# Kernel tuning notes

Measured on AMD Instinct MI355X. Metric: run time of the kernel, lower is better.

## Reference

```python
import jax, jax.numpy as jnp
import numpy as np

D_MODEL = 512
DQ = D_MODEL // 4  # 128
TIME_SHIFT_START = 256
VELOCITY_START = 768
NOTE_OFF_START = 128


def conv1d(x, w, b, stride, pad):
    # x: [B, Cin, L], w: [Cout, Cin, K]
    y = jax.lax.conv_general_dilated(x, w, (stride,), [(pad, pad)],
                                     dimension_numbers=('NCH', 'OIH', 'NCH'))
    return y + b[None, :, None]


def adaptive_avg_pool1d(x, out_size):
    # faithful to torch AdaptiveAvgPool1d bin boundaries
    L = x.shape[-1]
    starts = (np.arange(out_size) * L) // out_size
    ends = np.ceil((np.arange(out_size) + 1) * L / out_size).astype(np.int64)
    cs = jnp.concatenate([jnp.zeros(x.shape[:-1] + (1,), x.dtype),
                          jnp.cumsum(x, axis=-1)], axis=-1)
    return (cs[..., ends] - cs[..., starts]) / jnp.asarray(ends - starts, x.dtype)


def setup_inputs() -> dict:
    key = jax.random.key(0)
    ks = jax.random.split(key, 20)

    def w(k, shape):
        fan_in = int(np.prod(shape[1:]))
        return jax.random.normal(k, shape, jnp.float32) / np.sqrt(fan_in)

    def b(k, n):
        return jax.random.normal(k, (n,), jnp.float32) * 0.01

    return {
        'tokens': jax.random.randint(ks[0], (32, 4096), 0, 774),
        'r1_w': w(ks[1], (32, 1, 8)),    'r1_b': b(ks[2], 32),
        'r2_w': w(ks[3], (64, 32, 4)),   'r2_b': b(ks[4], 64),
        'h1_w': w(ks[5], (64, 128, 12)), 'h1_b': b(ks[6], 64),
        'h2_w': w(ks[7], (32, 64, 8)),   'h2_b': b(ks[8], 32),
        'm1_w': w(ks[9], (64, 128, 5)),  'm1_b': b(ks[10], 64),
        'm2_w': w(ks[11], (32, 64, 3)),  'm2_b': b(ks[12], 32),
        'd1_w': w(ks[13], (16, 6, 4)),   'd1_b': b(ks[14], 16),
        'd2_w': w(ks[15], (16, 16, 3)),  'd2_b': b(ks[16], 16),
        'fc_w': w(ks[17], (D_MODEL, D_MODEL)), 'fc_b': b(ks[18], D_MODEL),
    }


def reference(tokens, r1_w, r1_b, r2_w, r2_b, h1_w, h1_b, h2_w, h2_b,
              m1_w, m1_b, m2_w, m2_b, d1_w, d1_b, d2_w, d2_b, fc_w, fc_b):
    B, S = tokens.shape
    relu = jax.nn.relu

    # rhythm: binary time-shift indicator [B,1,S]
    ts = ((tokens >= TIME_SHIFT_START) & (tokens < VELOCITY_START)).astype(jnp.float32)[:, None, :]
    r = relu(conv1d(ts, r1_w, r1_b, 2, 3))
    r = relu(conv1d(r, r2_w, r2_b, 2, 1))
    r = adaptive_avg_pool1d(r, DQ).reshape(B, -1)  # [B, 64*DQ]

    # vectorized one-hot pitch scatter (replaces the python double loop): [B,128,S]
    nm = tokens < NOTE_OFF_START
    pitch = jnp.transpose(
        jax.nn.one_hot(jnp.where(nm, tokens, 0) % 128, 128, dtype=jnp.float32)
        * nm[..., None].astype(jnp.float32), (0, 2, 1))

    h = relu(conv1d(pitch, h1_w, h1_b, 1, 6))
    h = relu(conv1d(h, h2_w, h2_b, 2, 3))
    h = adaptive_avg_pool1d(h, DQ).reshape(B, -1)  # [B, 32*DQ]

    m = relu(conv1d(pitch, m1_w, m1_b, 1, 2))
    m = relu(conv1d(m, m2_w, m2_b, 1, 1))
    m = adaptive_avg_pool1d(m, DQ).reshape(B, -1)  # [B, 32*DQ]

    # velocity one-hot scatter: [B,6,S]
    vm = tokens >= VELOCITY_START
    vel = jnp.clip(jnp.where(vm, tokens - VELOCITY_START, 0), 0, 5)
    vpat = jnp.transpose(
        jax.nn.one_hot(vel, 6, dtype=jnp.float32) * vm[..., None].astype(jnp.float32),
        (0, 2, 1))
    d = relu(conv1d(vpat, d1_w, d1_b, 1, 2))
    d = relu(conv1d(d, d2_w, d2_b, 1, 1))
    d = adaptive_avg_pool1d(d, DQ).reshape(B, -1)  # [B, 16*DQ]

    # total flattened size is 36*d_model != d_model, so torch branch always pools
    r, h, m, d = [adaptive_avg_pool1d(f[:, None, :], DQ)[:, 0] for f in (r, h, m, d)]

    combined = jnp.concatenate([r, h, m, d], axis=1)       # [B, d_model]
    feats = combined @ fc_w.T + fc_b                        # Linear
    return jnp.broadcast_to(feats[:, None, :], (B, S, D_MODEL))
```

## Files before the change

### kernel.cpp

```cpp
#include <hip/hip_runtime.h>

typedef unsigned short u16;
typedef unsigned int u32;
typedef float vf4 __attribute__((ext_vector_type(4)));
typedef unsigned int vu4 __attribute__((ext_vector_type(4)));
typedef short sh8 __attribute__((ext_vector_type(8)));
typedef float f32x4 __attribute__((ext_vector_type(4)));

__device__ __forceinline__ float bf2f(u16 u) {
  return __uint_as_float(((u32)u) << 16);
}
__device__ __forceinline__ u16 f2bf(float f) {
  u32 x = __float_as_uint(f);
  return (u16)((x + 0x7fffu + ((x >> 16) & 1u)) >> 16);
}
__device__ __forceinline__ float ldin(const void* p, int idx, int isf) {
  return isf ? ((const float*)p)[idx] : bf2f(((const u16*)p)[idx]);
}

#define OFF_FLAG  ((size_t)0)
#define OFF_WB    ((size_t)16)
#define OFF_WTH1  ((size_t)1180432)
#define OFF_WTM1  ((size_t)1573648)
#define OFF_COMB  ((size_t)1737488)
#define OFF_FEATF ((size_t)1803024)
#define OFF_FEATB ((size_t)1868560)
#define OFF_DP    ((size_t)18686736)
#define OFF_WH2B  ((size_t)52536080)
#define OFF_WH2L  ((size_t)52568848)
#define OFF_WM2B  ((size_t)52601616)
#define OFF_WM2L  ((size_t)52613904)
#define WS_NEEDED ((size_t)52626192)

#define WB_R1W 0
#define WB_R1B 256
#define WB_R2W 288
#define WB_R2B 8480
#define WB_H1B 8544
#define WB_H2W 8608
#define WB_H2B 24992
#define WB_M1B 25024
#define WB_M2W 25088
#define WB_M2B 31232
#define WB_D1W 31264
#define WB_D1B 31648
#define WB_D2W 31664
#define WB_D2B 32432
#define WB_FCW 32448
#define WB_FCB 294592
#define WB_TOTAL 295104

__global__ __launch_bounds__(256) void k_convert(
    const void* r1_w, const void* r1_b, const void* r2_w, const void* r2_b,
    const void* h1_w, const void* h1_b, const void* h2_w, const void* h2_b,
    const void* m1_w, const void* m1_b, const void* m2_w, const void* m2_b,
    const void* d1_w, const void* d1_b, const void* d2_w, const void* d2_b,
    const void* fc_w, const void* fc_b,
    int* __restrict__ flagp, float* __restrict__ wb,
    float* __restrict__ wTh1, float* __restrict__ wTm1,
    float* __restrict__ combined,
    u16* __restrict__ wh2b, u16* __restrict__ wh2l,
    u16* __restrict__ wm2b, u16* __restrict__ wm2l) {
  __shared__ int cnt[4];
  int tid = threadIdx.x;
  {
    u16 v = ((const u16*)fc_w)[2 * tid];
    int e = (v >> 7) & 0xFF;
    int outside = (e < 100 || e > 140) ? 1 : 0;
    unsigned long long m = __ballot(outside);
    if ((tid & 63) == 0) cnt[tid >> 6] = __popcll(m);
  }
  __syncthreads();
  int isf = (cnt[0] + cnt[1] + cnt[2] + cnt[3] >= 64) ? 1 : 0;
  if (blockIdx.x == 0 && tid == 0) flagp[0] = isf;

  int j = blockIdx.x * 256 + tid;
  if (j >= 473280) return;
  if (j < WB_TOTAL) {
    const void* src; int si;
    if      (j < WB_R1B) { src = r1_w; si = j; }
    else if (j < WB_R2W) { src = r1_b; si = j - WB_R1B; }
    else if (j < WB_R2B) { src = r2_w; si = j - WB_R2W; }
    else if (j < WB_H1B) { src = r2_b; si = j - WB_R2B; }
    else if (j < WB_H2W) { src = h1_b; si = j - WB_H1B; }
    else if (j < WB_H2B) { src = h2_w; si = j - WB_H2W; }
    else if (j < WB_M1B) { src = h2_b; si = j - WB_H2B; }
    else if (j < WB_M2W) { src = m1_b; si = j - WB_M1B; }
    else if (j < WB_M2B) { src = m2_w; si = j - WB_M2W; }
    else if (j < WB_D1W) { src = m2_b; si = j - WB_M2B; }
    else if (j < WB_D1B) { src = d1_w; si = j - WB_D1W; }
    else if (j < WB_D2W) { src = d1_b; si = j - WB_D1B; }
    else if (j < WB_D2B) { src = d2_w; si = j - WB_D2W; }
    else if (j < WB_FCW) { src = d2_b; si = j - WB_D2B; }
    else if (j < WB_FCB) { src = fc_w; si = j - WB_FCW; }
    else                 { src = fc_b; si = j - WB_FCB; }
    wb[j] = ldin(src, si, isf);
  } else if (j < 393408) {
    int j2 = j - WB_TOTAL;
    int o = j2 & 63, r = j2 >> 6, k = r % 12, p = r / 12;
    wTh1[j2] = ldin(h1_w, (o * 128 + p) * 12 + k, isf);
  } else if (j < 434368) {
    int j3 = j - 393408;
    int o = j3 & 63, r = j3 >> 6, k = r % 5, p = r / 5;
    wTm1[j3] = ldin(m1_w, (o * 128 + p) * 5 + k, isf);
  } else if (j < 450752) {
    combined[j - 434368] = 0.f;
  } else if (j < 467136) {
    int jj = j - 450752;
    int o = jj >> 9, rem = jj & 511, c = rem >> 3, kk = rem & 7;
    float w = ldin(h2_w, (o * 64 + c) * 8 + kk, isf);
    u16 hi = f2bf(w);
    wh2b[jj] = hi;
    wh2l[jj] = f2bf(w - bf2f(hi));
  } else {
    int jj = j - 467136;
    int o = jj / 192, rem = jj % 192, c = rem / 3, kk = rem % 3;
    float w = ldin(m2_w, (o * 64 + c) * 3 + kk, isf);
    u16 hi = f2bf(w);
    wm2b[jj] = hi;
    wm2l[jj] = f2bf(w - bf2f(hi));
  }
}


#define HT_STRIDE 142
#define MT_STRIDE 265

__device__ __forceinline__ void dev_hf(float* smem, const int* tok,
                                       const float* wTh1, const float* h1bf,
                                       const u16* wh2b, const u16* wh2l,
                                       const float* h2bf,
                                       float* combined, int chunk, int q, int b) {
  u16* htile = (u16*)smem;
  int* tks = (int*)(smem + 4544);
  const int tid = threadIdx.x;
  const int tb = q * 512 + chunk * 64;
  const int sg0 = 2 * tb;
  const int* tokb = tok + b * 4096;
  if (tid < 146) {
    int x = sg0 - 9 + tid;
    tks[tid] = ((unsigned)x < 4096u) ? tokb[x] : 999;
  }
  __syncthreads();
  {
    const int og = tid & 15, slot = tid >> 4;
    const float4 bias = *(const float4*)(h1bf + og * 4);
    for (int pos = slot; pos < 134; pos += 16) {
      int t = sg0 - 3 + pos;
      u16 o0 = 0, o1 = 0, o2 = 0, o3 = 0;
      if ((unsigned)t <= 4096u) {
        float4 acc = bias;
#pragma unroll
        for (int k = 0; k < 12; ++k) {
          int p = tks[pos + k];
          if (p < 128) {
            float4 wv = *(const float4*)(wTh1 + (p * 12 + k) * 64 + og * 4);
            acc.x += wv.x; acc.y += wv.y; acc.z += wv.z; acc.w += wv.w;
          }
        }
        o0 = f2bf(fmaxf(acc.x, 0.f)); o1 = f2bf(fmaxf(acc.y, 0.f));
        o2 = f2bf(fmaxf(acc.z, 0.f)); o3 = f2bf(fmaxf(acc.w, 0.f));
      }
      int rb = og * 4 * HT_STRIDE + pos;
      htile[rb] = o0;
      htile[rb + HT_STRIDE] = o1;
      htile[rb + 2 * HT_STRIDE] = o2;
      htile[rb + 3 * HT_STRIDE] = o3;
    }
  }
  __syncthreads();
  const int w = tid >> 6, l = tid & 63;
  const int quad = l >> 4, n = l & 15;
  const int ot = w & 1, tp = w >> 1;
  f32x4 acc2[2];
  acc2[0] = (f32x4){0.f, 0.f, 0.f, 0.f};
  acc2[1] = (f32x4){0.f, 0.f, 0.f, 0.f};
  const u16* wph = wh2b + (size_t)(16 * ot + n) * 512 + quad * 8;
  const u16* wpl = wh2l + (size_t)(16 * ot + n) * 512 + quad * 8;
  const u32* hp = (const u32*)htile;
  for (int kc = 0; kc < 2; ++kc) {
    sh8 ah[8], al[8];
#pragma unroll
    for (int s = 0; s < 8; ++s) {
      ah[s] = *(const sh8*)(wph + kc * 256 + 32 * s);
      al[s] = *(const sh8*)(wpl + kc * 256 + 32 * s);
    }
#pragma unroll
    for (int it = 0; it < 2; ++it) {
      int fb = 16 * (2 * it + tp) + n;
#pragma unroll
      for (int s = 0; s < 8; ++s) {
        int c = kc * 32 + 4 * s + quad;
        const u32* p = hp + c * 71 + fb;
        u32 bw[4] = {p[0], p[1], p[2], p[3]};
        sh8 bb;
        __builtin_memcpy(&bb, bw, 16);
        acc2[it] = __builtin_amdgcn_mfma_f32_16x16x32_bf16(ah[s], bb, acc2[it], 0, 0, 0);
        acc2[it] = __builtin_amdgcn_mfma_f32_16x16x32_bf16(al[s], bb, acc2[it], 0, 0, 0);
      }
    }
  }
#pragma unroll
  for (int r = 0; r < 4; ++r) {
    float bsv = h2bf[16 * ot + quad * 4 + r];
    float s = fmaxf(acc2[0][r] + bsv, 0.f) + fmaxf(acc2[1][r] + bsv, 0.f);
    s += __shfl_xor(s, 1, 64);
    s += __shfl_xor(s, 2, 64);
    s += __shfl_xor(s, 4, 64);
    s += __shfl_xor(s, 8, 64);
    if (n == 0) {
      int o = 16 * ot + quad * 4 + r;
      atomicAdd(&combined[b * 512 + 128 + 4 * o + q], s * (1.f / 512.f));
    }
  }
}

__device__ __forceinline__ void dev_mf(float* smem, const int* tok,
                                       const float* wTm1, const float* m1bf,
                                       const u16* wm2b, const u16* wm2l,
                                       const float* m2bf,
                                       float* combined, int sub, int q, int b) {
  u16* mtile = (u16*)smem;
  int* tks = (int*)(smem + 8480);
  const int tid = threadIdx.x;
  const int tb = q * 1024 + sub * 256;
  const int* tokb = tok + b * 4096;
  for (int i = tid; i < 266; i += 256) {
    int x = tb - 4 + i;
    tks[i] = ((unsigned)x < 4096u) ? tokb[x] : 999;
  }
  __syncthreads();
  {
    const int og = tid & 15, slot = tid >> 4;
    const float4 bias = *(const float4*)(m1bf + og * 4);
    for (int u = slot; u < 262; u += 16) {
      int t = tb - 2 + u;
      u16 o0 = 0, o1 = 0, o2 = 0, o3 = 0;
      if ((unsigned)t < 4096u) {
        float4 acc = bias;
#pragma unroll
        for (int k = 0; k < 5; ++k) {
          int p = tks[u + k];
          if (p < 128) {
            float4 wv = *(const float4*)(wTm1 + (p * 5 + k) * 64 + og * 4);
            acc.x += wv.x; acc.y += wv.y; acc.z += wv.z; acc.w += wv.w;
          }
        }
        o0 = f2bf(fmaxf(acc.x, 0.f)); o1 = f2bf(fmaxf(acc.y, 0.f));
        o2 = f2bf(fmaxf(acc.z, 0.f)); o3 = f2bf(fmaxf(acc.w, 0.f));
      }
      int rb = og * 4 * MT_STRIDE + u;
      mtile[rb] = o0;
      mtile[rb + MT_STRIDE] = o1;
      mtile[rb + 2 * MT_STRIDE] = o2;
      mtile[rb + 3 * MT_STRIDE] = o3;
    }
  }
  __syncthreads();
  const int w = tid >> 6, l = tid & 63;
  const int quad = l >> 4, n = l & 15;
  const int ot = w & 1, tp = w >> 1;
  sh8 ah[6], al[6];
  {
    const u16* wph = wm2b + (size_t)(16 * ot + n) * 192 + quad * 8;
    const u16* wpl = wm2l + (size_t)(16 * ot + n) * 192 + quad * 8;
#pragma unroll
    for (int s = 0; s < 6; ++s) {
      ah[s] = *(const sh8*)(wph + 32 * s);
      al[s] = *(const sh8*)(wpl + 32 * s);
    }
  }
  float bsv[4];
#pragma unroll
  for (int r = 0; r < 4; ++r) bsv[r] = m2bf[16 * ot + quad * 4 + r];
  float sm[4] = {0.f, 0.f, 0.f, 0.f};
  const int gkb = quad * 8;
  for (int it = 0; it < 8; ++it) {
    int ub = 16 * (2 * it + tp) + n + 1;
    f32x4 acc = {0.f, 0.f, 0.f, 0.f};
#pragma unroll
    for (int s = 0; s < 6; ++s) {
      sh8 bb;
#pragma unroll
      for (int j = 0; j < 8; ++j) {
        int gk = 32 * s + gkb + j;
        int c = (gk * 21846) >> 16;
        int kk = gk - 3 * c;
        bb[j] = (short)mtile[c * MT_STRIDE + ub + kk];
      }
      acc = __builtin_amdgcn_mfma_f32_16x16x32_bf16(ah[s], bb, acc, 0, 0, 0);
      acc = __builtin_amdgcn_mfma_f32_16x16x32_bf16(al[s], bb, acc, 0, 0, 0);
    }
#pragma unroll
    for (int r = 0; r < 4; ++r) sm[r] += fmaxf(acc[r] + bsv[r], 0.f);
  }
#pragma unroll
  for (int r = 0; r < 4; ++r) {
    float s = sm[r];
    s += __shfl_xor(s, 1, 64);
    s += __shfl_xor(s, 2, 64);
    s += __shfl_xor(s, 4, 64);
    s += __shfl_xor(s, 8, 64);
    if (n == 0) {
      int o = 16 * ot + quad * 4 + r;
      atomicAdd(&combined[b * 512 + 256 + 4 * o + q], s * (1.f / 1024.f));
    }
  }
}

__device__ __forceinline__ void dev_rf(float* smem, const int* tok,
                                       const float* r1wf, const float* r1bf,
                                       const float* r2wf, const float* r2bf,
                                       float* combined, int chunk, int b) {
  float* w1s = smem;
  float* b1s = smem + 256;
  float* Ibuf = smem + 288;
  float* r1t = smem + 560;
  float* wcr = smem + 4848;
  const int tid = threadIdx.x;
  const int tbase = chunk * 64;
  const int tk0 = 4 * tbase - 7;
  const int* tokb = tok + b * 4096;
  w1s[tid] = r1wf[tid];
  if (tid < 32) b1s[tid] = r1bf[tid];
  for (int i = tid; i < 270; i += 256) {
    int x = tk0 + i;
    float v = 0.f;
    if ((unsigned)x < 4096u) {
      int tk = tokb[x];
      v = (tk >= 256 && tk < 768) ? 1.f : 0.f;
    }
    Ibuf[i] = v;
  }
  __syncthreads();
  {
    const int tl1 = tid & 63, og1 = tid >> 6;
    for (int xi = tl1; xi < 134; xi += 64) {
      int x = 2 * tbase - 2 + xi;
      if ((unsigned)x < 2048u) {
        float iv[8];
#pragma unroll
        for (int k = 0; k < 8; ++k) iv[k] = Ibuf[2 * xi + k];
#pragma unroll
        for (int i = 0; i < 8; ++i) {
          int o = og1 * 8 + i;
          float a = b1s[o];
#pragma unroll
          for (int k = 0; k < 8; ++k) a = fmaf(w1s[o * 8 + k], iv[k], a);
          r1t[o * 134 + xi] = fmaxf(a, 0.f);
        }
      } else {
#pragma unroll
        for (int i = 0; i < 8; ++i) r1t[(og1 * 8 + i) * 134 + xi] = 0.f;
      }
    }
  }
  __syncthreads();
  const int half = chunk >> 3;
  const int og = tid >> 6, tl = tid & 63;
  float acc[16];
#pragma unroll
  for (int i = 0; i < 16; ++i) acc[i] = 0.f;
  for (int c0 = 0; c0 < 32; c0 += 8) {
    for (int f = tid; f < 2048; f += 256) {
      int o = f & 63, r = f >> 6, k = r & 3, cc = r >> 2;
      wcr[f] = r2wf[(o * 32 + c0 + cc) * 4 + k];
    }
    __syncthreads();
#pragma unroll
    for (int cc = 0; cc < 8; ++cc) {
      const float* rr = r1t + (c0 + cc) * 134 + 2 * tl;
      float ev[3], od[3];
#pragma unroll
      for (int f3 = 0; f3 < 3; ++f3) {
        ev[f3] = rr[2 * f3];
        od[f3] = rr[2 * f3 + 1];
      }
#pragma unroll
      for (int k = 0; k < 4; ++k) {
        const int p = (k + 1) & 1, fk = (k + 1) >> 1;
        const float* wv = &wcr[(cc * 4 + k) * 64 + og * 16];
        float4 wa = *(const float4*)wv;
        float4 wbv = *(const float4*)(wv + 4);
        float4 wcc = *(const float4*)(wv + 8);
        float4 wd4 = *(const float4*)(wv + 12);
        float wr[16] = {wa.x, wa.y, wa.z, wa.w, wbv.x, wbv.y, wbv.z, wbv.w,
                        wcc.x, wcc.y, wcc.z, wcc.w, wd4.x, wd4.y, wd4.z, wd4.w};
        float v0 = p ? od[fk] : ev[fk];
#pragma unroll
        for (int i = 0; i < 16; ++i) acc[i] = fmaf(v0, wr[i], acc[i]);
      }
    }
    __syncthreads();
  }
  const float inv = 1.f / 512.f;
#pragma unroll
  for (int i = 0; i < 16; ++i) {
    int o = og * 16 + i;
    float s = fmaxf(acc[i] + r2bf[o], 0.f);
#pragma unroll
    for (int d = 32; d > 0; d >>= 1) s += __shfl_down(s, d, 64);
    if (tl == 0) atomicAdd(&combined[b * 512 + 2 * o + half], s * inv);
  }
}

__device__ __forceinline__ void dev_df(float* smem, const int* tok,
                                       const float* d1wf, const float* d1bf,
                                       const float* d2wf, const float* d2bf,
                                       float* dpws, int chunk, int b) {
  float* wds = smem;
  float* wd = smem + 384;
  int* cls = (int*)(smem + 1152);
  float (*dt)[132] = reinterpret_cast<float(*)[132]>(smem + 1288);
  float* c2 = smem + 3400;
  const int tid = threadIdx.x;
  const int tbase = chunk * 128;
  const int* tokb = tok + b * 4096;
  for (int f = tid; f < 384; f += 256) wds[f] = d1wf[f];
  for (int f = tid; f < 768; f += 256) wd[f] = d2wf[f];
  if (tid < 136) {
    int x = tbase - 3 + tid;
    int v = -1;
    if ((unsigned)x < 4096u) {
      int tk = tokb[x];
      if (tk >= 768) { v = tk - 768; v = v > 5 ? 5 : v; }
    }
    cls[tid] = v;
  }
  __syncthreads();
  for (int f = tid; f < 16 * 131; f += 256) {
    int iu = f % 131, c = f / 131;
    int x = tbase - 1 + iu;
    float v = 0.f;
    if (x >= 0 && x <= 4096) {
      float a = d1bf[c];
#pragma unroll
      for (int k = 0; k < 4; ++k) {
        int vc = cls[iu + k];
        if (vc >= 0) a += wds[(c * 6 + vc) * 4 + k];
      }
      v = fmaxf(a, 0.f);
    }
    dt[c][iu] = v;
  }
  __syncthreads();
  for (int idx = tid; idx < 16 * 129; idx += 256) {
    int o = idx / 129, tl = idx % 129;
    float a = d2bf[o];
    const float* ww = &wd[o * 48];
#pragma unroll 4
    for (int c = 0; c < 16; ++c) {
      a = fmaf(dt[c][tl], ww[c * 3 + 0],
          fmaf(dt[c][tl + 1], ww[c * 3 + 1],
          fmaf(dt[c][tl + 2], ww[c * 3 + 2], a)));
    }
    c2[o * 133 + tl] = fmaxf(a, 0.f);
  }
  __syncthreads();
  if (tid < 64) {
    int o = tid >> 2, qq = tid & 3;
    const float* row = c2 + o * 133 + 32 * qq;
    float s = 0.f;
#pragma unroll
    for (int j = 0; j < 33; ++j) s += row[j];
    dpws[(size_t)(b * 16 + o) * 128 + 4 * chunk + qq] = s * (1.f / 33.f);
  }
}

__global__ __launch_bounds__(256, 4) void k_fused(const int* __restrict__ tok,
                                                  const float* __restrict__ wb,
                                                  const float* __restrict__ wTh1,
                                                  const float* __restrict__ wTm1,
                                                  const u16* __restrict__ wh2b,
                                                  const u16* __restrict__ wh2l,
                                                  const u16* __restrict__ wm2b,
                                                  const u16* __restrict__ wm2l,
                                                  float* __restrict__ combined,
                                                  float* __restrict__ dpws) {
  __shared__ __align__(16) float smem[8752];
  int bx = blockIdx.x;
  if (bx < 1024) {
    dev_hf(smem, tok, wTh1, wb + WB_H1B, wh2b, wh2l, wb + WB_H2B, combined,
           bx & 7, (bx >> 3) & 3, bx >> 5);
  } else if (bx < 1536) {
    int n = bx - 1024;
    dev_mf(smem, tok, wTm1, wb + WB_M1B, wm2b, wm2l, wb + WB_M2B, combined,
           n & 3, (n >> 2) & 3, n >> 4);
  } else if (bx < 2048) {
    int n = bx - 1536;
    dev_rf(smem, tok, wb + WB_R1W, wb + WB_R1B, wb + WB_R2W, wb + WB_R2B,
           combined, n & 15, n >> 4);
  } else {
    int n = bx - 2048;
    dev_df(smem, tok, wb + WB_D1W, wb + WB_D1B, wb + WB_D2W, wb + WB_D2B,
           dpws, n & 31, n >> 5);
  }
}

__global__ __launch_bounds__(256) void k_fc(const float* __restrict__ combined,
                                            const float* __restrict__ dpws,
                                            const float* __restrict__ fcwf,
                                            const float* __restrict__ fcbf,
                                            float* __restrict__ featf,
                                            u16* __restrict__ featb) {
  const int bx = blockIdx.x;
  const int b = bx >> 3, oct = bx & 7;
  const int tid = threadIdx.x;
  __shared__ float cb[512];
  cb[tid] = combined[b * 512 + tid];
  if (tid < 128) {
    cb[256 + tid] = combined[b * 512 + 256 + tid];
  } else {
    int j = tid - 128;
    int o = j >> 3, i0 = (j & 7) * 16;
    const float* row = dpws + (size_t)(b * 16 + o) * 128;
    float s = 0.f;
#pragma unroll
    for (int i = 0; i < 16; ++i) s += row[i0 + i];
    cb[384 + j] = s * (1.f / 16.f);
  }
  __syncthreads();
  const int oo = oct * 64 + (tid >> 2), part = tid & 3;
  float acc = 0.f;
  const float4* wr = (const float4*)(fcwf + (size_t)oo * 512 + part * 128);
#pragma unroll 8
  for (int j4 = 0; j4 < 32; ++j4) {
    float4 w = wr[j4];
    const float* c4 = &cb[part * 128 + j4 * 4];
    acc = fmaf(c4[0], w.x, acc);
    acc = fmaf(c4[1], w.y, acc);
    acc = fmaf(c4[2], w.z, acc);
    acc = fmaf(c4[3], w.w, acc);
  }
  acc += __shfl_xor(acc, 1, 64);
  acc += __shfl_xor(acc, 2, 64);
  if (part == 0) {
    float r = acc + fcbf[oo];
    featf[b * 512 + oo] = r;
    featb[b * 512 + oo] = f2bf(r);
  }
}

__global__ __launch_bounds__(256) void k_bcast(const int* __restrict__ flagp,
                                               const vf4* __restrict__ featf4,
                                               const vu4* __restrict__ featb4,
                                               vf4* __restrict__ outf,
                                               vu4* __restrict__ outb) {
  if (flagp[0]) {
    int base = blockIdx.x * 1024 + threadIdx.x;
#pragma unroll
    for (int s = 0; s < 4; ++s) {
      int g = base + s * 256;
      vf4 v = featf4[(g >> 19) * 128 + (g & 127)];
      __builtin_nontemporal_store(v, &outf[g]);
    }
  } else {
    int base = blockIdx.x * 512 + threadIdx.x;
#pragma unroll
    for (int s = 0; s < 2; ++s) {
      int g = base + s * 256;
      vu4 v = featb4[(g >> 18) * 64 + (g & 63)];
      __builtin_nontemporal_store(v, &outb[g]);
    }
  }
}

extern "C" void kernel_launch(void* const* d_in, const int* in_sizes, int n_in,
                              void* d_out, int out_size, void* d_ws, size_t ws_size,
                              hipStream_t stream) {
  if (ws_size < WS_NEEDED) return;

  const int* tokens = (const int*)d_in[0];
  const void* r1_w = d_in[1];  const void* r1_b = d_in[2];
  const void* r2_w = d_in[3];  const void* r2_b = d_in[4];
  const void* h1_w = d_in[5];  const void* h1_b = d_in[6];
  const void* h2_w = d_in[7];  const void* h2_b = d_in[8];
  const void* m1_w = d_in[9];  const void* m1_b = d_in[10];
  const void* m2_w = d_in[11]; const void* m2_b = d_in[12];
  const void* d1_w = d_in[13]; const void* d1_b = d_in[14];
  const void* d2_w = d_in[15]; const void* d2_b = d_in[16];
  const void* fc_w = d_in[17]; const void* fc_b = d_in[18];

  char* ws = (char*)d_ws;
  int*   flagp   = (int*)  (ws + OFF_FLAG);
  float* wb      = (float*)(ws + OFF_WB);
  float* wTh1    = (float*)(ws + OFF_WTH1);
  float* wTm1    = (float*)(ws + OFF_WTM1);
  float* combined= (float*)(ws + OFF_COMB);
  float* featf   = (float*)(ws + OFF_FEATF);
  u16*   featb   = (u16*)  (ws + OFF_FEATB);
  float* dpws    = (float*)(ws + OFF_DP);
  u16*   wh2b    = (u16*)  (ws + OFF_WH2B);
  u16*   wh2l    = (u16*)  (ws + OFF_WH2L);
  u16*   wm2b    = (u16*)  (ws + OFF_WM2B);
  u16*   wm2l    = (u16*)  (ws + OFF_WM2L);

  k_convert<<<1849, 256, 0, stream>>>(r1_w, r1_b, r2_w, r2_b, h1_w, h1_b, h2_w, h2_b,
                                      m1_w, m1_b, m2_w, m2_b, d1_w, d1_b, d2_w, d2_b,
                                      fc_w, fc_b, flagp, wb, wTh1, wTm1, combined,
                                      wh2b, wh2l, wm2b, wm2l);
  k_fused<<<3072, 256, 0, stream>>>(tokens, wb, wTh1, wTm1, wh2b, wh2l, wm2b, wm2l,
                                    combined, dpws);
  k_fc<<<256, 256, 0, stream>>>(combined, dpws, wb + WB_FCW, wb + WB_FCB, featf, featb);
  k_bcast<<<16384, 256, 0, stream>>>(flagp, (const vf4*)featf, (const vu4*)featb,
                                     (vf4*)d_out, (vu4*)d_out);
}
```

Measured before the change: 392.2 us.

## Halve m-branch tiles, stream MFMA weights, raise occupancy to five blocks

The m-branch block now covers 128 timesteps instead of 256, doubling its block count and shrinking shared memory so the fused kernel can request five blocks per CU. Weight fragments for the h2 and m2 MFMAs are loaded from global memory inside the loop rather than kept in register arrays, which lowers register pressure. This trades extra halo recomputation and repeated weight loads for higher occupancy and better load balance across the fused grid.

```diff
diff --git a/kernel.cpp b/kernel.cpp
--- a/kernel.cpp
+++ b/kernel.cpp
@@ -124,7 +124,7 @@
 
 
 #define HT_STRIDE 142
-#define MT_STRIDE 265
+#define MT_STRIDE 133
 
 __device__ __forceinline__ void dev_hf(float* smem, const int* tok,
                                        const float* wTh1, const float* h1bf,
@@ -179,24 +179,20 @@
   const u16* wpl = wh2l + (size_t)(16 * ot + n) * 512 + quad * 8;
   const u32* hp = (const u32*)htile;
   for (int kc = 0; kc < 2; ++kc) {
-    sh8 ah[8], al[8];
-#pragma unroll
-    for (int s = 0; s < 8; ++s) {
-      ah[s] = *(const sh8*)(wph + kc * 256 + 32 * s);
-      al[s] = *(const sh8*)(wpl + kc * 256 + 32 * s);
-    }
 #pragma unroll
     for (int it = 0; it < 2; ++it) {
       int fb = 16 * (2 * it + tp) + n;
 #pragma unroll
       for (int s = 0; s < 8; ++s) {
+        sh8 ah = *(const sh8*)(wph + kc * 256 + 32 * s);
+        sh8 al = *(const sh8*)(wpl + kc * 256 + 32 * s);
         int c = kc * 32 + 4 * s + quad;
         const u32* p = hp + c * 71 + fb;
         u32 bw[4] = {p[0], p[1], p[2], p[3]};
         sh8 bb;
         __builtin_memcpy(&bb, bw, 16);
-        acc2[it] = __builtin_amdgcn_mfma_f32_16x16x32_bf16(ah[s], bb, acc2[it], 0, 0, 0);
-        acc2[it] = __builtin_amdgcn_mfma_f32_16x16x32_bf16(al[s], bb, acc2[it], 0, 0, 0);
+        acc2[it] = __builtin_amdgcn_mfma_f32_16x16x32_bf16(ah, bb, acc2[it], 0, 0, 0);
+        acc2[it] = __builtin_amdgcn_mfma_f32_16x16x32_bf16(al, bb, acc2[it], 0, 0, 0);
       }
     }
   }
@@ -221,19 +217,19 @@
                                        const float* m2bf,
                                        float* combined, int sub, int q, int b) {
   u16* mtile = (u16*)smem;
-  int* tks = (int*)(smem + 8480);
+  int* tks = (int*)(smem + 4256);
   const int tid = threadIdx.x;
-  const int tb = q * 1024 + sub * 256;
+  const int tb = q * 1024 + sub * 128;
   const int* tokb = tok + b * 4096;
-  for (int i = tid; i < 266; i += 256) {
-    int x = tb - 4 + i;
-    tks[i] = ((unsigned)x < 4096u) ? tokb[x] : 999;
+  if (tid < 135) {
+    int x = tb - 4 + tid;
+    tks[tid] = ((unsigned)x < 4096u) ? tokb[x] : 999;
   }
   __syncthreads();
   {
     const int og = tid & 15, slot = tid >> 4;
     const float4 bias = *(const float4*)(m1bf + og * 4);
-    for (int u = slot; u < 262; u += 16) {
+    for (int u = slot; u < 131; u += 16) {
       int t = tb - 2 + u;
       u16 o0 = 0, o1 = 0, o2 = 0, o3 = 0;
       if ((unsigned)t < 4096u) {
@@ -260,26 +256,20 @@
   const int w = tid >> 6, l = tid & 63;
   const int quad = l >> 4, n = l & 15;
   const int ot = w & 1, tp = w >> 1;
-  sh8 ah[6], al[6];
-  {
-    const u16* wph = wm2b + (size_t)(16 * ot + n) * 192 + quad * 8;
-    const u16* wpl = wm2l + (size_t)(16 * ot + n) * 192 + quad * 8;
-#pragma unroll
-    for (int s = 0; s < 6; ++s) {
-      ah[s] = *(const sh8*)(wph + 32 * s);
-      al[s] = *(const sh8*)(wpl + 32 * s);
-    }
-  }
+  const u16* wph = wm2b + (size_t)(16 * ot + n) * 192 + quad * 8;
+  const u16* wpl = wm2l + (size_t)(16 * ot + n) * 192 + quad * 8;
   float bsv[4];
 #pragma unroll
   for (int r = 0; r < 4; ++r) bsv[r] = m2bf[16 * ot + quad * 4 + r];
   float sm[4] = {0.f, 0.f, 0.f, 0.f};
   const int gkb = quad * 8;
-  for (int it = 0; it < 8; ++it) {
+  for (int it = 0; it < 4; ++it) {
     int ub = 16 * (2 * it + tp) + n + 1;
     f32x4 acc = {0.f, 0.f, 0.f, 0.f};
 #pragma unroll
     for (int s = 0; s < 6; ++s) {
+      sh8 ah = *(const sh8*)(wph + 32 * s);
+      sh8 al = *(const sh8*)(wpl + 32 * s);
       sh8 bb;
 #pragma unroll
       for (int j = 0; j < 8; ++j) {
@@ -288,8 +278,8 @@
         int kk = gk - 3 * c;
         bb[j] = (short)mtile[c * MT_STRIDE + ub + kk];
       }
-      acc = __builtin_amdgcn_mfma_f32_16x16x32_bf16(ah[s], bb, acc, 0, 0, 0);
-      acc = __builtin_amdgcn_mfma_f32_16x16x32_bf16(al[s], bb, acc, 0, 0, 0);
+      acc = __builtin_amdgcn_mfma_f32_16x16x32_bf16(ah, bb, acc, 0, 0, 0);
+      acc = __builtin_amdgcn_mfma_f32_16x16x32_bf16(al, bb, acc, 0, 0, 0);
     }
 #pragma unroll
     for (int r = 0; r < 4; ++r) sm[r] += fmaxf(acc[r] + bsv[r], 0.f);
@@ -467,7 +457,7 @@
   }
 }
 
-__global__ __launch_bounds__(256, 4) void k_fused(const int* __restrict__ tok,
+__global__ __launch_bounds__(256, 5) void k_fused(const int* __restrict__ tok,
                                                   const float* __restrict__ wb,
                                                   const float* __restrict__ wTh1,
                                                   const float* __restrict__ wTm1,
@@ -477,21 +467,21 @@
                                                   const u16* __restrict__ wm2l,
                                                   float* __restrict__ combined,
                                                   float* __restrict__ dpws) {
-  __shared__ __align__(16) float smem[8752];
+  __shared__ __align__(16) float smem[6896];
   int bx = blockIdx.x;
   if (bx < 1024) {
     dev_hf(smem, tok, wTh1, wb + WB_H1B, wh2b, wh2l, wb + WB_H2B, combined,
            bx & 7, (bx >> 3) & 3, bx >> 5);
-  } else if (bx < 1536) {
+  } else if (bx < 2048) {
     int n = bx - 1024;
     dev_mf(smem, tok, wTm1, wb + WB_M1B, wm2b, wm2l, wb + WB_M2B, combined,
-           n & 3, (n >> 2) & 3, n >> 4);
-  } else if (bx < 2048) {
-    int n = bx - 1536;
+           n & 7, (n >> 3) & 3, n >> 5);
+  } else if (bx < 2560) {
+    int n = bx - 2048;
     dev_rf(smem, tok, wb + WB_R1W, wb + WB_R1B, wb + WB_R2W, wb + WB_R2B,
            combined, n & 15, n >> 4);
   } else {
-    int n = bx - 2048;
+    int n = bx - 2560;
     dev_df(smem, tok, wb + WB_D1W, wb + WB_D1B, wb + WB_D2W, wb + WB_D2B,
            dpws, n & 31, n >> 5);
   }
@@ -599,7 +589,7 @@
                                       m1_w, m1_b, m2_w, m2_b, d1_w, d1_b, d2_w, d2_b,
                                       fc_w, fc_b, flagp, wb, wTh1, wTm1, combined,
                                       wh2b, wh2l, wm2b, wm2l);
-  k_fused<<<3072, 256, 0, stream>>>(tokens, wb, wTh1, wTm1, wh2b, wh2l, wm2b, wm2l,
+  k_fused<<<3584, 256, 0, stream>>>(tokens, wb, wTh1, wTm1, wh2b, wh2l, wm2b, wm2l,
                                     combined, dpws);
   k_fc<<<256, 256, 0, stream>>>(combined, dpws, wb + WB_FCW, wb + WB_FCB, featf, featb);
   k_bcast<<<16384, 256, 0, stream>>>(flagp, (const vf4*)featf, (const vu4*)featb,
```

Measured after the change: 398.1 us. Within noise of the previous version (+1.5%).

## Make conv gathers branchless with zero-padded weight rows and halve m-branch tiles

Applied to the files above, without the earlier changes.

The first-layer pitch and velocity gathers now index a weight table with an appended zero row, so non-matching tokens add zeros instead of taking a branch. Token indices are pre-multiplied into offsets in shared memory. The m-branch work is split into twice as many blocks, each covering half the positions, which reduces shared memory per block and may allow higher occupancy. The cost is extra loads for padding tokens and more blocks in the launch.

```diff
diff --git a/kernel.cpp b/kernel.cpp
--- a/kernel.cpp
+++ b/kernel.cpp
@@ -21,10 +21,10 @@
 #define OFF_FLAG  ((size_t)0)
 #define OFF_WB    ((size_t)16)
 #define OFF_WTH1  ((size_t)1180432)
-#define OFF_WTM1  ((size_t)1573648)
-#define OFF_COMB  ((size_t)1737488)
-#define OFF_FEATF ((size_t)1803024)
-#define OFF_FEATB ((size_t)1868560)
+#define OFF_WTM1  ((size_t)1576720)
+#define OFF_COMB  ((size_t)1741840)
+#define OFF_FEATF ((size_t)1807376)
+#define OFF_FEATB ((size_t)1872912)
 #define OFF_DP    ((size_t)18686736)
 #define OFF_WH2B  ((size_t)52536080)
 #define OFF_WH2L  ((size_t)52568848)
@@ -49,6 +49,12 @@
 #define WB_FCW 32448
 #define WB_FCB 294592
 #define WB_TOTAL 295104
+
+#define CV_TH1_END 394176
+#define CV_TM1_END 435456
+#define CV_CMB_END 451840
+#define CV_WH2_END 468224
+#define CV_TOTAL   474368
 
 __global__ __launch_bounds__(256) void k_convert(
     const void* r1_w, const void* r1_b, const void* r2_w, const void* r2_b,
@@ -75,7 +81,7 @@
   if (blockIdx.x == 0 && tid == 0) flagp[0] = isf;
 
   int j = blockIdx.x * 256 + tid;
-  if (j >= 473280) return;
+  if (j >= CV_TOTAL) return;
   if (j < WB_TOTAL) {
     const void* src; int si;
     if      (j < WB_R1B) { src = r1_w; si = j; }
@@ -95,25 +101,25 @@
     else if (j < WB_FCB) { src = fc_w; si = j - WB_FCW; }
     else                 { src = fc_b; si = j - WB_FCB; }
     wb[j] = ldin(src, si, isf);
-  } else if (j < 393408) {
+  } else if (j < CV_TH1_END) {
     int j2 = j - WB_TOTAL;
-    int o = j2 & 63, r = j2 >> 6, k = r % 12, p = r / 12;
-    wTh1[j2] = ldin(h1_w, (o * 128 + p) * 12 + k, isf);
-  } else if (j < 434368) {
-    int j3 = j - 393408;
-    int o = j3 & 63, r = j3 >> 6, k = r % 5, p = r / 5;
-    wTm1[j3] = ldin(m1_w, (o * 128 + p) * 5 + k, isf);
-  } else if (j < 450752) {
-    combined[j - 434368] = 0.f;
-  } else if (j < 467136) {
-    int jj = j - 450752;
+    int o = j2 & 63, r = j2 >> 6;
+    wTh1[j2] = (r >= 1536) ? 0.f : ldin(h1_w, (o * 128 + r / 12) * 12 + (r % 12), isf);
+  } else if (j < CV_TM1_END) {
+    int j3 = j - CV_TH1_END;
+    int o = j3 & 63, r = j3 >> 6;
+    wTm1[j3] = (r >= 640) ? 0.f : ldin(m1_w, (o * 128 + r / 5) * 5 + (r % 5), isf);
+  } else if (j < CV_CMB_END) {
+    combined[j - CV_TM1_END] = 0.f;
+  } else if (j < CV_WH2_END) {
+    int jj = j - CV_CMB_END;
     int o = jj >> 9, rem = jj & 511, c = rem >> 3, kk = rem & 7;
     float w = ldin(h2_w, (o * 64 + c) * 8 + kk, isf);
     u16 hi = f2bf(w);
     wh2b[jj] = hi;
     wh2l[jj] = f2bf(w - bf2f(hi));
   } else {
-    int jj = j - 467136;
+    int jj = j - CV_WH2_END;
     int o = jj / 192, rem = jj % 192, c = rem / 3, kk = rem % 3;
     float w = ldin(m2_w, (o * 64 + c) * 3 + kk, isf);
     u16 hi = f2bf(w);
@@ -124,7 +130,7 @@
 
 
 #define HT_STRIDE 142
-#define MT_STRIDE 265
+#define MT_STRIDE 133
 
 __device__ __forceinline__ void dev_hf(float* smem, const int* tok,
                                        const float* wTh1, const float* h1bf,
@@ -139,12 +145,14 @@
   const int* tokb = tok + b * 4096;
   if (tid < 146) {
     int x = sg0 - 9 + tid;
-    tks[tid] = ((unsigned)x < 4096u) ? tokb[x] : 999;
+    int p = ((unsigned)x < 4096u) ? tokb[x] : 128;
+    tks[tid] = (p < 128 ? p : 128) * 768;
   }
   __syncthreads();
   {
     const int og = tid & 15, slot = tid >> 4;
     const float4 bias = *(const float4*)(h1bf + og * 4);
+    const float* wbase = wTh1 + og * 4;
     for (int pos = slot; pos < 134; pos += 16) {
       int t = sg0 - 3 + pos;
       u16 o0 = 0, o1 = 0, o2 = 0, o3 = 0;
@@ -152,11 +160,8 @@
         float4 acc = bias;
 #pragma unroll
         for (int k = 0; k < 12; ++k) {
-          int p = tks[pos + k];
-          if (p < 128) {
-            float4 wv = *(const float4*)(wTh1 + (p * 12 + k) * 64 + og * 4);
-            acc.x += wv.x; acc.y += wv.y; acc.z += wv.z; acc.w += wv.w;
-          }
+          const float4 wv = *(const float4*)(wbase + tks[pos + k] + k * 64);
+          acc.x += wv.x; acc.y += wv.y; acc.z += wv.z; acc.w += wv.w;
         }
         o0 = f2bf(fmaxf(acc.x, 0.f)); o1 = f2bf(fmaxf(acc.y, 0.f));
         o2 = f2bf(fmaxf(acc.z, 0.f)); o3 = f2bf(fmaxf(acc.w, 0.f));
@@ -221,30 +226,29 @@
                                        const float* m2bf,
                                        float* combined, int sub, int q, int b) {
   u16* mtile = (u16*)smem;
-  int* tks = (int*)(smem + 8480);
+  int* tks = (int*)(smem + 4256);
   const int tid = threadIdx.x;
-  const int tb = q * 1024 + sub * 256;
+  const int tb = q * 1024 + sub * 128;
   const int* tokb = tok + b * 4096;
-  for (int i = tid; i < 266; i += 256) {
-    int x = tb - 4 + i;
-    tks[i] = ((unsigned)x < 4096u) ? tokb[x] : 999;
+  if (tid < 135) {
+    int x = tb - 4 + tid;
+    int p = ((unsigned)x < 4096u) ? tokb[x] : 128;
+    tks[tid] = (p < 128 ? p : 128) * 320;
   }
   __syncthreads();
   {
     const int og = tid & 15, slot = tid >> 4;
     const float4 bias = *(const float4*)(m1bf + og * 4);
-    for (int u = slot; u < 262; u += 16) {
+    const float* wbase = wTm1 + og * 4;
+    for (int u = slot; u < 131; u += 16) {
       int t = tb - 2 + u;
       u16 o0 = 0, o1 = 0, o2 = 0, o3 = 0;
       if ((unsigned)t < 4096u) {
         float4 acc = bias;
 #pragma unroll
         for (int k = 0; k < 5; ++k) {
-          int p = tks[u + k];
-          if (p < 128) {
-            float4 wv = *(const float4*)(wTm1 + (p * 5 + k) * 64 + og * 4);
-            acc.x += wv.x; acc.y += wv.y; acc.z += wv.z; acc.w += wv.w;
-          }
+          const float4 wv = *(const float4*)(wbase + tks[u + k] + k * 64);
+          acc.x += wv.x; acc.y += wv.y; acc.z += wv.z; acc.w += wv.w;
         }
         o0 = f2bf(fmaxf(acc.x, 0.f)); o1 = f2bf(fmaxf(acc.y, 0.f));
         o2 = f2bf(fmaxf(acc.z, 0.f)); o3 = f2bf(fmaxf(acc.w, 0.f));
@@ -275,7 +279,7 @@
   for (int r = 0; r < 4; ++r) bsv[r] = m2bf[16 * ot + quad * 4 + r];
   float sm[4] = {0.f, 0.f, 0.f, 0.f};
   const int gkb = quad * 8;
-  for (int it = 0; it < 8; ++it) {
+  for (int it = 0; it < 4; ++it) {
     int ub = 16 * (2 * it + tp) + n + 1;
     f32x4 acc = {0.f, 0.f, 0.f, 0.f};
 #pragma unroll
@@ -408,22 +412,25 @@
                                        const float* d1wf, const float* d1bf,
                                        const float* d2wf, const float* d2bf,
                                        float* dpws, int chunk, int b) {
-  float* wds = smem;
-  float* wd = smem + 384;
-  int* cls = (int*)(smem + 1152);
-  float (*dt)[132] = reinterpret_cast<float(*)[132]>(smem + 1288);
-  float* c2 = smem + 3400;
+  float* wds7 = smem;
+  float* wd = smem + 448;
+  int* cls = (int*)(smem + 1216);
+  float (*dt)[132] = reinterpret_cast<float(*)[132]>(smem + 1352);
+  float* c2 = smem + 3464;
   const int tid = threadIdx.x;
   const int tbase = chunk * 128;
   const int* tokb = tok + b * 4096;
-  for (int f = tid; f < 384; f += 256) wds[f] = d1wf[f];
+  for (int f = tid; f < 448; f += 256) {
+    int k = f & 3, rest = f >> 2, v = rest % 7, c = rest / 7;
+    wds7[f] = (v < 6) ? d1wf[(c * 6 + v) * 4 + k] : 0.f;
+  }
   for (int f = tid; f < 768; f += 256) wd[f] = d2wf[f];
   if (tid < 136) {
     int x = tbase - 3 + tid;
-    int v = -1;
+    int v = 6;
     if ((unsigned)x < 4096u) {
       int tk = tokb[x];
-      if (tk >= 768) { v = tk - 768; v = v > 5 ? 5 : v; }
+      if (tk >= 768) { v = tk - 768; v = v > 5 ? 5 : v; } else v = 6;
     }
     cls[tid] = v;
   }
@@ -436,8 +443,7 @@
       float a = d1bf[c];
 #pragma unroll
       for (int k = 0; k < 4; ++k) {
-        int vc = cls[iu + k];
-        if (vc >= 0) a += wds[(c * 6 + vc) * 4 + k];
+        a += wds7[(c * 7 + cls[iu + k]) * 4 + k];
       }
       v = fmaxf(a, 0.f);
     }
@@ -477,21 +483,21 @@
                                                   const u16* __restrict__ wm2l,
                                                   float* __restrict__ combined,
                                                   float* __restrict__ dpws) {
-  __shared__ __align__(16) float smem[8752];
+  __shared__ __align__(16) float smem[6896];
   int bx = blockIdx.x;
   if (bx < 1024) {
     dev_hf(smem, tok, wTh1, wb + WB_H1B, wh2b, wh2l, wb + WB_H2B, combined,
            bx & 7, (bx >> 3) & 3, bx >> 5);
-  } else if (bx < 1536) {
+  } else if (bx < 2048) {
     int n = bx - 1024;
     dev_mf(smem, tok, wTm1, wb + WB_M1B, wm2b, wm2l, wb + WB_M2B, combined,
-           n & 3, (n >> 2) & 3, n >> 4);
-  } else if (bx < 2048) {
-    int n = bx - 1536;
+           n & 7, (n >> 3) & 3, n >> 5);
+  } else if (bx < 2560) {
+    int n = bx - 2048;
     dev_rf(smem, tok, wb + WB_R1W, wb + WB_R1B, wb + WB_R2W, wb + WB_R2B,
            combined, n & 15, n >> 4);
   } else {
-    int n = bx - 2048;
+    int n = bx - 2560;
     dev_df(smem, tok, wb + WB_D1W, wb + WB_D1B, wb + WB_D2W, wb + WB_D2B,
            dpws, n & 31, n >> 5);
   }
@@ -595,11 +601,11 @@
   u16*   wm2b    = (u16*)  (ws + OFF_WM2B);
   u16*   wm2l    = (u16*)  (ws + OFF_WM2L);
 
-  k_convert<<<1849, 256, 0, stream>>>(r1_w, r1_b, r2_w, r2_b, h1_w, h1_b, h2_w, h2_b,
+  k_convert<<<1853, 256, 0, stream>>>(r1_w, r1_b, r2_w, r2_b, h1_w, h1_b, h2_w, h2_b,
                                       m1_w, m1_b, m2_w, m2_b, d1_w, d1_b, d2_w, d2_b,
                                       fc_w, fc_b, flagp, wb, wTh1, wTm1, combined,
                                       wh2b, wh2l, wm2b, wm2l);
-  k_fused<<<3072, 256, 0, stream>>>(tokens, wb, wTh1, wTm1, wh2b, wh2l, wm2b, wm2l,
+  k_fused<<<3584, 256, 0, stream>>>(tokens, wb, wTh1, wTm1, wh2b, wh2l, wm2b, wm2l,
                                     combined, dpws);
   k_fc<<<256, 256, 0, stream>>>(combined, dpws, wb + WB_FCW, wb + WB_FCB, featf, featb);
   k_bcast<<<16384, 256, 0, stream>>>(flagp, (const vf4*)featf, (const vu4*)featb,
```

After: 392.3 us. No clear change (+0.0%).
